# Kernel tuning notes

Hardware: AMD Instinct MI355X
Metric: run time of the kernel (lower is better)

Reference implementation:

```python
import jax, jax.numpy as jnp
import numpy as np

B, C, H, W = 16, 128, 128, 128
NUM_HEADS, HEAD_DIM = 4, 32
HIDDEN = NUM_HEADS * HEAD_DIM  # 128
GROUPS = 32
EPS = 1e-5


def setup_inputs() -> dict:
    key = jax.random.key(0)
    ks = jax.random.split(key, 6)
    # conv1x1 weights: torch Conv2d weight (out, in, 1, 1) -> stored as (out, in)
    fan_qkv = C
    fan_proj = HIDDEN
    return {
        "x": jax.random.normal(ks[0], (B, C, H, W), dtype=jnp.float32),
        "gn_w": jnp.ones((C,), dtype=jnp.float32),
        "gn_b": jnp.zeros((C,), dtype=jnp.float32),
        "qkv_w": jax.random.normal(ks[1], (3 * HIDDEN, C), dtype=jnp.float32) / np.sqrt(fan_qkv),
        "proj_w": jax.random.normal(ks[2], (C, HIDDEN), dtype=jnp.float32) / np.sqrt(fan_proj),
        "proj_b": jax.random.normal(ks[3], (C,), dtype=jnp.float32) * 0.01,
    }


def reference(x, gn_w, gn_b, qkv_w, proj_w, proj_b):
    b, c, h, w = x.shape
    n = h * w
    residual = x
    # GroupNorm(32 groups), biased variance, affine
    xg = x.reshape(b, GROUPS, c // GROUPS, h, w)
    mu = xg.mean(axis=(2, 3, 4), keepdims=True)
    var = xg.var(axis=(2, 3, 4), keepdims=True)
    xn = ((xg - mu) * jax.lax.rsqrt(var + EPS)).reshape(b, c, h, w)
    xn = xn * gn_w[None, :, None, None] + gn_b[None, :, None, None]
    # 1x1 conv QKV (no bias); channel layout -> (b, 3, heads, head_dim, n)
    qkv = jnp.einsum('oc,bchw->bohw', qkv_w, xn)
    qkv = qkv.reshape(b, 3, NUM_HEADS, HEAD_DIM, n)
    q, k, v = qkv[:, 0], qkv[:, 1], qkv[:, 2]
    q = jax.nn.softmax(q, axis=-1)   # over spatial positions
    k = jax.nn.softmax(k, axis=-2)   # over head_dim
    # context = k @ v^T : (b,h,D,D)
    ctx = jnp.einsum('bhdn,bhen->bhde', k, v)
    # out = context^T @ q : (b,h,D,n)
    out = jnp.einsum('bhde,bhdn->bhen', ctx, q)
    out = out.reshape(b, HIDDEN, h, w)
    # 1x1 conv projection (with bias)
    out = jnp.einsum('co,bohw->bchw', proj_w, out) + proj_b[None, :, None, None]
    return out + residual
```

## Files before the change

kernel.cpp:

```cpp
#include <hip/hip_runtime.h>


#define B_ 16
#define C_ 128
#define N_ 16384

typedef short bf16x8 __attribute__((ext_vector_type(8)));
typedef float f32x4 __attribute__((ext_vector_type(4)));
typedef unsigned u32x2 __attribute__((ext_vector_type(2)));

__device__ __forceinline__ ushort f2bf(float f) {
    union { float f; unsigned u; } v; v.f = f;
    unsigned r = (v.u + 0x7FFFu + ((v.u >> 16) & 1u)) >> 16;
    return (ushort)r;
}
__device__ __forceinline__ float bf2f(unsigned h) {
    union { unsigned u; float f; } v; v.u = h << 16;
    return v.f;
}

__global__ void k_pack(const float* __restrict__ w, ushort* __restrict__ wbf, int n) {
    int i = blockIdx.x * 256 + threadIdx.x;
    if (i < n) wbf[i] = f2bf(w[i]);
}

__global__ void k_stats(const float* __restrict__ x, const float* __restrict__ gnw,
                        const float* __restrict__ gnb, float* __restrict__ sc,
                        float* __restrict__ bi) {
    int bg = blockIdx.x;
    const float4* p = (const float4*)(x + (size_t)bg * (4 * N_));
    float s = 0.f, s2 = 0.f;
    for (int i = threadIdx.x; i < N_; i += 1024) {
        float4 v = p[i];
        s  += v.x + v.y + v.z + v.w;
        s2 += v.x * v.x + v.y * v.y + v.z * v.z + v.w * v.w;
    }
    #pragma unroll
    for (int d = 32; d > 0; d >>= 1) { s += __shfl_xor(s, d); s2 += __shfl_xor(s2, d); }
    __shared__ float ls[16], ls2[16];
    int wid = threadIdx.x >> 6, lane = threadIdx.x & 63;
    if (lane == 0) { ls[wid] = s; ls2[wid] = s2; }
    __syncthreads();
    if (threadIdx.x == 0) {
        float S = 0.f, S2 = 0.f;
        #pragma unroll
        for (int i = 0; i < 16; ++i) { S += ls[i]; S2 += ls2[i]; }
        float m = S / 65536.f;
        float var = S2 / 65536.f - m * m;
        float rs = rsqrtf(var + 1e-5f);
        int b = bg >> 5, g = bg & 31;
        #pragma unroll
        for (int i = 0; i < 4; ++i) {
            int c = g * 4 + i;
            float scv = rs * gnw[c];
            sc[b * 128 + c] = scv;
            bi[b * 128 + c] = gnb[c] - m * scv;
        }
    }
}


#define MFMA16(A, Bv, Cc) __builtin_amdgcn_mfma_f32_16x16x32_bf16(A, Bv, Cc, 0, 0, 0)

#define DO_Q(J, OT) do { \
    f32x4 acc = {0.f, 0.f, 0.f, 0.f}; \
    acc = MFMA16(wf[J][0], xb[0], acc); acc = MFMA16(wf[J][1], xb[1], acc); \
    acc = MFMA16(wf[J][2], xb[2], acc); acc = MFMA16(wf[J][3], xb[3], acc); \
    float e0 = __expf(acc[0]), e1 = __expf(acc[1]); \
    float e2 = __expf(acc[2]), e3 = __expf(acc[3]); \
    qacc[J][0] += e0; qacc[J][1] += e1; qacc[J][2] += e2; qacc[J][3] += e3; \
    u32x2 pkq; \
    pkq.x = (unsigned)f2bf(e0) | ((unsigned)f2bf(e1) << 16); \
    pkq.y = (unsigned)f2bf(e2) | ((unsigned)f2bf(e3) << 16); \
    *(u32x2*)(eqp + (OT) * 16) = pkq; \
} while (0)

#define DO_K(JLO, H) do { \
    f32x4 aL = {0.f, 0.f, 0.f, 0.f}, aH = {0.f, 0.f, 0.f, 0.f}; \
    aL = MFMA16(wf[JLO][0], xb[0], aL);     aH = MFMA16(wf[(JLO)+1][0], xb[0], aH); \
    aL = MFMA16(wf[JLO][1], xb[1], aL);     aH = MFMA16(wf[(JLO)+1][1], xb[1], aH); \
    aL = MFMA16(wf[JLO][2], xb[2], aL);     aH = MFMA16(wf[(JLO)+1][2], xb[2], aH); \
    aL = MFMA16(wf[JLO][3], xb[3], aL);     aH = MFMA16(wf[(JLO)+1][3], xb[3], aH); \
    float eL0 = __expf(aL[0]), eL1 = __expf(aL[1]), eL2 = __expf(aL[2]), eL3 = __expf(aL[3]); \
    float eH0 = __expf(aH[0]), eH1 = __expf(aH[1]), eH2 = __expf(aH[2]), eH3 = __expf(aH[3]); \
    float s = eL0 + eL1 + eL2 + eL3 + eH0 + eH1 + eH2 + eH3; \
    s += __shfl_xor(s, 16); s += __shfl_xor(s, 32); \
    float rinv = 1.f / s; \
    ksm[H][lg * 4 + 0][nloc] = f2bf(eL0 * rinv); \
    ksm[H][lg * 4 + 1][nloc] = f2bf(eL1 * rinv); \
    ksm[H][lg * 4 + 2][nloc] = f2bf(eL2 * rinv); \
    ksm[H][lg * 4 + 3][nloc] = f2bf(eL3 * rinv); \
    ksm[H][16 + lg * 4 + 0][nloc] = f2bf(eH0 * rinv); \
    ksm[H][16 + lg * 4 + 1][nloc] = f2bf(eH1 * rinv); \
    ksm[H][16 + lg * 4 + 2][nloc] = f2bf(eH2 * rinv); \
    ksm[H][16 + lg * 4 + 3][nloc] = f2bf(eH3 * rinv); \
} while (0)

#define DO_V(J, HV, EB) do { \
    f32x4 acc = {0.f, 0.f, 0.f, 0.f}; \
    acc = MFMA16(wf[J][0], xb[0], acc); acc = MFMA16(wf[J][1], xb[1], acc); \
    acc = MFMA16(wf[J][2], xb[2], acc); acc = MFMA16(wf[J][3], xb[3], acc); \
    vls[HV][(EB) + lg * 4 + 0][nloc] = f2bf(acc[0]); \
    vls[HV][(EB) + lg * 4 + 1][nloc] = f2bf(acc[1]); \
    vls[HV][(EB) + lg * 4 + 2][nloc] = f2bf(acc[2]); \
    vls[HV][(EB) + lg * 4 + 3][nloc] = f2bf(acc[3]); \
} while (0)

__global__ __launch_bounds__(256, 2) void k_main(
    const float* __restrict__ x, const ushort* __restrict__ wbf,
    const float* __restrict__ scA, const float* __restrict__ biA,
    ushort* __restrict__ eqT, float* __restrict__ qsumP, float* __restrict__ ctxP) {
    int blk = blockIdx.x;
    int b = blk >> 6, nb = blk & 63;
    int tid = threadIdx.x, wid = tid >> 6, lane = tid & 63;
    int l15 = lane & 15, lg = lane >> 4;

    __shared__ __align__(16) ushort xs[8192];
    __shared__ __align__(16) ushort ksm[4][32][72];
    __shared__ __align__(16) ushort vls[4][32][72];

    bf16x8 wf[6][4];
    {
        const ushort* wr = wbf + (size_t)(wid * 96 + l15) * 128 + lg * 8;
        #pragma unroll
        for (int j = 0; j < 6; ++j)
            #pragma unroll
            for (int kc = 0; kc < 4; ++kc)
                wf[j][kc] = *(const bf16x8*)(wr + j * 2048 + kc * 32);
    }

    float qacc[6][4];
    #pragma unroll
    for (int j = 0; j < 6; ++j)
        #pragma unroll
        for (int r = 0; r < 4; ++r) qacc[j][r] = 0.f;
    f32x4 cacc[2][2];
    #pragma unroll
    for (int di = 0; di < 2; ++di)
        #pragma unroll
        for (int ei = 0; ei < 2; ++ei) cacc[di][ei] = (f32x4){0.f, 0.f, 0.f, 0.f};

    const int pk_ = tid & 15, pcb = tid >> 4;
    const float* xrow = x + (size_t)b * (C_ * N_) + nb * 256 + pk_ * 4;
    float scv[8], biv[8];
    #pragma unroll
    for (int i = 0; i < 8; ++i) {
        scv[i] = scA[b * 128 + pcb * 8 + i];
        biv[i] = biA[b * 128 + pcb * 8 + i];
    }
    unsigned boffj[4];
    #pragma unroll
    for (int j = 0; j < 4; ++j) {
        int n = pk_ * 4 + j;
        boffj[j] = (unsigned)(n * 256 + ((pcb * 16) ^ ((n & 7) << 4)));
    }

    for (int ch = 0; ch < 4; ++ch) {
        union { uint4 v; unsigned w[4]; } wj0, wj1, wj2, wj3;
        #pragma unroll
        for (int i = 0; i < 8; ++i) {
            float4 v = *(const float4*)(xrow + (size_t)(pcb * 8 + i) * N_ + ch * 64);
            float s = scv[i], t = biv[i];
            unsigned e0 = f2bf(v.x * s + t), e1 = f2bf(v.y * s + t);
            unsigned e2 = f2bf(v.z * s + t), e3 = f2bf(v.w * s + t);
            int wI = i >> 1;
            if (i & 1) {
                wj0.w[wI] |= e0 << 16; wj1.w[wI] |= e1 << 16;
                wj2.w[wI] |= e2 << 16; wj3.w[wI] |= e3 << 16;
            } else {
                wj0.w[wI] = e0; wj1.w[wI] = e1; wj2.w[wI] = e2; wj3.w[wI] = e3;
            }
        }
        *(uint4*)((char*)xs + boffj[0]) = wj0.v;
        *(uint4*)((char*)xs + boffj[1]) = wj1.v;
        *(uint4*)((char*)xs + boffj[2]) = wj2.v;
        *(uint4*)((char*)xs + boffj[3]) = wj3.v;
        __syncthreads();

        for (int nt = 0; nt < 4; ++nt) {
            int row = nt * 16 + l15;
            bf16x8 xb[4];
            #pragma unroll
            for (int kc = 0; kc < 4; ++kc) {
                unsigned off = (unsigned)(row * 256 +
                    (((kc * 4 + lg) * 16) ^ ((row & 7) << 4)));
                xb[kc] = *(const bf16x8*)((const char*)xs + off);
            }
            int nloc = nt * 16 + l15;
            int ng = nb * 256 + ch * 64 + nloc;
            ushort* eqp = eqT + ((size_t)b * N_ + ng) * 128 + lg * 4;

            if (wid == 0) {
                DO_Q(0, 0); DO_Q(1, 1); DO_Q(2, 2); DO_Q(3, 3); DO_Q(4, 4); DO_Q(5, 5);
            } else if (wid == 1) {
                DO_Q(0, 6); DO_Q(1, 7); DO_K(2, 0); DO_K(4, 1);
            } else if (wid == 2) {
                DO_K(0, 2); DO_K(2, 3); DO_V(4, 0, 0); DO_V(5, 0, 16);
            } else {
                DO_V(0, 1, 0); DO_V(1, 1, 16); DO_V(2, 2, 0);
                DO_V(3, 2, 16); DO_V(4, 3, 0); DO_V(5, 3, 16);
            }
        }
        __syncthreads();

        #pragma unroll
        for (int ks = 0; ks < 2; ++ks) {
            bf16x8 A0 = *(const bf16x8*)&ksm[wid][l15][ks * 32 + lg * 8];
            bf16x8 A1 = *(const bf16x8*)&ksm[wid][16 + l15][ks * 32 + lg * 8];
            bf16x8 B0 = *(const bf16x8*)&vls[wid][l15][ks * 32 + lg * 8];
            bf16x8 B1 = *(const bf16x8*)&vls[wid][16 + l15][ks * 32 + lg * 8];
            cacc[0][0] = MFMA16(A0, B0, cacc[0][0]);
            cacc[0][1] = MFMA16(A0, B1, cacc[0][1]);
            cacc[1][0] = MFMA16(A1, B0, cacc[1][0]);
            cacc[1][1] = MFMA16(A1, B1, cacc[1][1]);
        }
        __syncthreads();
    }

    int nq = (wid == 0) ? 6 : (wid == 1 ? 2 : 0);
    #pragma unroll
    for (int j = 0; j < 6; ++j) {
        if (j < nq) {
            #pragma unroll
            for (int r = 0; r < 4; ++r) {
                float s = qacc[j][r];
                s += __shfl_xor(s, 1); s += __shfl_xor(s, 2);
                s += __shfl_xor(s, 4); s += __shfl_xor(s, 8);
                if (l15 == 0)
                    qsumP[(size_t)blk * 128 + (wid * 6 + j) * 16 + lg * 4 + r] = s;
            }
        }
    }
    float* cp = ctxP + (size_t)blk * 4096 + wid * 1024;
    #pragma unroll
    for (int di = 0; di < 2; ++di)
        #pragma unroll
        for (int ei = 0; ei < 2; ++ei)
            #pragma unroll
            for (int r = 0; r < 4; ++r)
                cp[(di * 16 + lg * 4 + r) * 32 + ei * 16 + l15] = cacc[di][ei][r];
}

__global__ void k_red(float* __restrict__ ctxP) {
    int blk = blockIdx.x;
    int b = blk >> 3, sl = blk & 7;
    float* base = ctxP + (size_t)b * 64 * 4096;
    #pragma unroll
    for (int r = 0; r < 2; ++r) {
        int i = sl * 512 + r * 256 + threadIdx.x;
        float s = 0.f;
        for (int q = 0; q < 64; ++q) s += base[(size_t)q * 4096 + i];
        base[i] = s;
    }
}

__global__ void k_comb(const float* __restrict__ ctxP, const float* __restrict__ qsumP,
                       const float* __restrict__ projw, ushort* __restrict__ mpp) {
    int b = blockIdx.x, tid = threadIdx.x;
    __shared__ float ctx[4096];
    __shared__ float qinv[128];
    for (int i = tid; i < 4096; i += 256)
        ctx[i] = ctxP[(size_t)b * 64 * 4096 + i];
    if (tid < 128) {
        float s = 0.f;
        const float* p = qsumP + (size_t)b * 64 * 128 + tid;
        for (int q = 0; q < 64; ++q) s += p[q * 128];
        qinv[tid] = 1.f / s;
    }
    __syncthreads();
    int c = tid >> 1, hd0 = (tid & 1) * 64;
    unsigned ow[32];
    for (int k = 0; k < 64; ++k) {
        int hd = hd0 + k, h = hd >> 5, d = hd & 31;
        const float* pw = projw + c * 128 + h * 32;
        const float* cx = ctx + h * 1024 + d * 32;
        float s = 0.f;
        #pragma unroll 8
        for (int e = 0; e < 32; ++e) s += pw[e] * cx[e];
        s *= qinv[hd];
        ushort bv = f2bf(s);
        if (k & 1) ow[k >> 1] |= ((unsigned)bv) << 16; else ow[k >> 1] = bv;
    }
    ushort* dst = mpp + ((size_t)(b * 128 + c)) * 128 + hd0;
    #pragma unroll
    for (int q = 0; q < 8; ++q) {
        uint4 t; t.x = ow[q * 4]; t.y = ow[q * 4 + 1]; t.z = ow[q * 4 + 2]; t.w = ow[q * 4 + 3];
        ((uint4*)dst)[q] = t;
    }
}

__global__ __launch_bounds__(256) void k_final(
    const ushort* __restrict__ eqT, const ushort* __restrict__ mpp,
    const float* __restrict__ projb, const float* __restrict__ x,
    float* __restrict__ out) {
    int blk = blockIdx.x;
    int b = blk >> 7, nb = blk & 127;
    int tid = threadIdx.x, wid = tid >> 6, lane = tid & 63;
    int l15 = lane & 15, lg = lane >> 4;

    __shared__ __align__(16) ushort att[16384];

    bf16x8 bm[2][4];
    #pragma unroll
    for (int ctk = 0; ctk < 2; ++ctk) {
        const ushort* br = mpp + ((size_t)(b * 128 + (wid * 2 + ctk) * 16 + l15)) * 128 + lg * 8;
        #pragma unroll
        for (int kc = 0; kc < 4; ++kc) bm[ctk][kc] = *(const bf16x8*)(br + kc * 32);
    }

    int n0 = nb * 128;
    #pragma unroll
    for (int nt = 0; nt < 8; ++nt) {
        const ushort* ar = eqT + ((size_t)b * N_ + n0 + nt * 16 + l15) * 128 + lg * 8;
        bf16x8 af[4];
        #pragma unroll
        for (int kc = 0; kc < 4; ++kc) af[kc] = *(const bf16x8*)(ar + kc * 32);
        #pragma unroll
        for (int ctk = 0; ctk < 2; ++ctk) {
            f32x4 a = {0.f, 0.f, 0.f, 0.f};
            #pragma unroll
            for (int kc = 0; kc < 4; ++kc) a = MFMA16(af[kc], bm[ctk][kc], a);
            int c = (wid * 2 + ctk) * 16 + l15;
            int nloc = nt * 16 + lg * 4;
            unsigned byte = (unsigned)(c * 256 + ((nloc * 2) ^ ((c & 15) << 4)));
            u32x2 pk;
            pk.x = (unsigned)f2bf(a[0]) | ((unsigned)f2bf(a[1]) << 16);
            pk.y = (unsigned)f2bf(a[2]) | ((unsigned)f2bf(a[3]) << 16);
            *(u32x2*)((char*)att + byte) = pk;
        }
    }
    __syncthreads();

    int crow = lane >> 5;
    int n4 = (lane & 31) * 4;
    #pragma unroll
    for (int it = 0; it < 16; ++it) {
        int c = wid * 32 + it * 2 + crow;
        unsigned byte = (unsigned)(c * 256 + ((n4 * 2) ^ ((c & 15) << 4)));
        u32x2 pk = *(const u32x2*)((const char*)att + byte);
        size_t off = (size_t)(b * C_ + c) * N_ + n0 + n4;
        f32x4 xv = __builtin_nontemporal_load((const f32x4*)(x + off));
        float pbv = projb[c];
        f32x4 o4;
        o4[0] = bf2f(pk.x & 0xffffu) + pbv + xv[0];
        o4[1] = bf2f(pk.x >> 16)     + pbv + xv[1];
        o4[2] = bf2f(pk.y & 0xffffu) + pbv + xv[2];
        o4[3] = bf2f(pk.y >> 16)     + pbv + xv[3];
        *(f32x4*)(out + off) = o4;
    }
}

extern "C" void kernel_launch(void* const* d_in, const int* in_sizes, int n_in,
                              void* d_out, int out_size, void* d_ws, size_t ws_size,
                              hipStream_t stream) {
    const float* x     = (const float*)d_in[0];
    const float* gnw   = (const float*)d_in[1];
    const float* gnb   = (const float*)d_in[2];
    const float* qkvw  = (const float*)d_in[3];
    const float* projw = (const float*)d_in[4];
    const float* projb = (const float*)d_in[5];
    float* out = (float*)d_out;

    char* ws = (char*)d_ws;
    ushort* wbf   = (ushort*)(ws);
    float*  qsumP = (float*)(ws + 102400);
    ushort* mpp   = (ushort*)(ws + 626688);
    float*  sc    = (float*)(ws + 626688);
    float*  bi    = (float*)(ws + 634880);
    float*  ctxP  = (float*)(ws + 1150976);
    ushort* eqT   = (ushort*)(ws + 17928192);

    k_pack <<<192,  256,  0, stream>>>(qkvw, wbf, 384 * 128);
    k_stats<<<512,  1024, 0, stream>>>(x, gnw, gnb, sc, bi);
    k_main <<<1024, 256,  0, stream>>>(x, wbf, sc, bi, eqT, qsumP, ctxP);
    k_red  <<<128,  256,  0, stream>>>(ctxP);
    k_comb <<<16,   256,  0, stream>>>(ctxP, qsumP, projw, mpp);
    k_final<<<2048, 256,  0, stream>>>(eqT, mpp, projb, x, out);
}
```

Baseline: 241.3 us.

## Fold weight packing into stats kernel and halve main-kernel LDS chunk size

The bf16 weight-packing kernel is merged into the GroupNorm stats kernel as extra blocks, removing one launch. The main kernel now processes 8 chunks of 32 positions instead of 4 chunks of 64, which roughly halves its LDS footprint (xs, ksm, vls) so more blocks can be resident per CU. The trailing barrier in each chunk is replaced by a barrier at the start of the next chunk. The cost is twice as many chunk iterations and barriers, with smaller global load batches per thread.

```diff
diff --git a/kernel.cpp b/kernel.cpp
--- a/kernel.cpp
+++ b/kernel.cpp
@@ -19,15 +19,16 @@
     return v.f;
 }
 
-__global__ void k_pack(const float* __restrict__ w, ushort* __restrict__ wbf, int n) {
-    int i = blockIdx.x * 256 + threadIdx.x;
-    if (i < n) wbf[i] = f2bf(w[i]);
-}
-
 __global__ void k_stats(const float* __restrict__ x, const float* __restrict__ gnw,
                         const float* __restrict__ gnb, float* __restrict__ sc,
-                        float* __restrict__ bi) {
+                        float* __restrict__ bi,
+                        const float* __restrict__ qkvw, ushort* __restrict__ wbf) {
     int bg = blockIdx.x;
+    if (bg >= 512) {
+        int i = (bg - 512) * 1024 + threadIdx.x;
+        if (i < 384 * 128) wbf[i] = f2bf(qkvw[i]);
+        return;
+    }
     const float4* p = (const float4*)(x + (size_t)bg * (4 * N_));
     float s = 0.f, s2 = 0.f;
     for (int i = threadIdx.x; i < N_; i += 1024) {
@@ -115,9 +116,9 @@
     int tid = threadIdx.x, wid = tid >> 6, lane = tid & 63;
     int l15 = lane & 15, lg = lane >> 4;
 
-    __shared__ __align__(16) ushort xs[8192];
-    __shared__ __align__(16) ushort ksm[4][32][72];
-    __shared__ __align__(16) ushort vls[4][32][72];
+    __shared__ __align__(16) ushort xs[4096];
+    __shared__ __align__(16) ushort ksm[4][32][40];
+    __shared__ __align__(16) ushort vls[4][32][40];
 
     bf16x8 wf[6][4];
     {
@@ -140,44 +141,44 @@
         #pragma unroll
         for (int ei = 0; ei < 2; ++ei) cacc[di][ei] = (f32x4){0.f, 0.f, 0.f, 0.f};
 
-    const int pk_ = tid & 15, pcb = tid >> 4;
+    const int pk_ = tid & 7, pcb = tid >> 3;
     const float* xrow = x + (size_t)b * (C_ * N_) + nb * 256 + pk_ * 4;
-    float scv[8], biv[8];
-    #pragma unroll
-    for (int i = 0; i < 8; ++i) {
-        scv[i] = scA[b * 128 + pcb * 8 + i];
-        biv[i] = biA[b * 128 + pcb * 8 + i];
+    float scv[4], biv[4];
+    #pragma unroll
+    for (int i = 0; i < 4; ++i) {
+        scv[i] = scA[b * 128 + pcb * 4 + i];
+        biv[i] = biA[b * 128 + pcb * 4 + i];
     }
     unsigned boffj[4];
     #pragma unroll
     for (int j = 0; j < 4; ++j) {
         int n = pk_ * 4 + j;
-        boffj[j] = (unsigned)(n * 256 + ((pcb * 16) ^ ((n & 7) << 4)));
-    }
-
-    for (int ch = 0; ch < 4; ++ch) {
-        union { uint4 v; unsigned w[4]; } wj0, wj1, wj2, wj3;
-        #pragma unroll
-        for (int i = 0; i < 8; ++i) {
-            float4 v = *(const float4*)(xrow + (size_t)(pcb * 8 + i) * N_ + ch * 64);
+        boffj[j] = (unsigned)(n * 256 + (((pcb >> 1) * 16) ^ ((n & 7) << 4)) + (pcb & 1) * 8);
+    }
+
+    for (int ch = 0; ch < 8; ++ch) {
+        __syncthreads();
+        unsigned e[4][4];
+        #pragma unroll
+        for (int i = 0; i < 4; ++i) {
+            float4 v = *(const float4*)(xrow + (size_t)(pcb * 4 + i) * N_ + ch * 32);
             float s = scv[i], t = biv[i];
-            unsigned e0 = f2bf(v.x * s + t), e1 = f2bf(v.y * s + t);
-            unsigned e2 = f2bf(v.z * s + t), e3 = f2bf(v.w * s + t);
-            int wI = i >> 1;
-            if (i & 1) {
-                wj0.w[wI] |= e0 << 16; wj1.w[wI] |= e1 << 16;
-                wj2.w[wI] |= e2 << 16; wj3.w[wI] |= e3 << 16;
-            } else {
-                wj0.w[wI] = e0; wj1.w[wI] = e1; wj2.w[wI] = e2; wj3.w[wI] = e3;
-            }
-        }
-        *(uint4*)((char*)xs + boffj[0]) = wj0.v;
-        *(uint4*)((char*)xs + boffj[1]) = wj1.v;
-        *(uint4*)((char*)xs + boffj[2]) = wj2.v;
-        *(uint4*)((char*)xs + boffj[3]) = wj3.v;
+            e[i][0] = f2bf(v.x * s + t);
+            e[i][1] = f2bf(v.y * s + t);
+            e[i][2] = f2bf(v.z * s + t);
+            e[i][3] = f2bf(v.w * s + t);
+        }
+        #pragma unroll
+        for (int j = 0; j < 4; ++j) {
+            u32x2 wj;
+            wj.x = e[0][j] | (e[1][j] << 16);
+            wj.y = e[2][j] | (e[3][j] << 16);
+            *(u32x2*)((char*)xs + boffj[j]) = wj;
+        }
         __syncthreads();
 
-        for (int nt = 0; nt < 4; ++nt) {
+        #pragma unroll
+        for (int nt = 0; nt < 2; ++nt) {
             int row = nt * 16 + l15;
             bf16x8 xb[4];
             #pragma unroll
@@ -187,7 +188,7 @@
                 xb[kc] = *(const bf16x8*)((const char*)xs + off);
             }
             int nloc = nt * 16 + l15;
-            int ng = nb * 256 + ch * 64 + nloc;
+            int ng = nb * 256 + ch * 32 + nloc;
             ushort* eqp = eqT + ((size_t)b * N_ + ng) * 128 + lg * 4;
 
             if (wid == 0) {
@@ -203,18 +204,16 @@
         }
         __syncthreads();
 
-        #pragma unroll
-        for (int ks = 0; ks < 2; ++ks) {
-            bf16x8 A0 = *(const bf16x8*)&ksm[wid][l15][ks * 32 + lg * 8];
-            bf16x8 A1 = *(const bf16x8*)&ksm[wid][16 + l15][ks * 32 + lg * 8];
-            bf16x8 B0 = *(const bf16x8*)&vls[wid][l15][ks * 32 + lg * 8];
-            bf16x8 B1 = *(const bf16x8*)&vls[wid][16 + l15][ks * 32 + lg * 8];
+        {
+            bf16x8 A0 = *(const bf16x8*)&ksm[wid][l15][lg * 8];
+            bf16x8 A1 = *(const bf16x8*)&ksm[wid][16 + l15][lg * 8];
+            bf16x8 B0 = *(const bf16x8*)&vls[wid][l15][lg * 8];
+            bf16x8 B1 = *(const bf16x8*)&vls[wid][16 + l15][lg * 8];
             cacc[0][0] = MFMA16(A0, B0, cacc[0][0]);
             cacc[0][1] = MFMA16(A0, B1, cacc[0][1]);
             cacc[1][0] = MFMA16(A1, B0, cacc[1][0]);
             cacc[1][1] = MFMA16(A1, B1, cacc[1][1]);
         }
-        __syncthreads();
     }
 
     int nq = (wid == 0) ? 6 : (wid == 1 ? 2 : 0);
@@ -370,8 +369,7 @@
     float*  ctxP  = (float*)(ws + 1150976);
     ushort* eqT   = (ushort*)(ws + 17928192);
 
-    k_pack <<<192,  256,  0, stream>>>(qkvw, wbf, 384 * 128);
-    k_stats<<<512,  1024, 0, stream>>>(x, gnw, gnb, sc, bi);
+    k_stats<<<560,  1024, 0, stream>>>(x, gnw, gnb, sc, bi, qkvw, wbf);
     k_main <<<1024, 256,  0, stream>>>(x, wbf, sc, bi, eqT, qsumP, ctxP);
     k_red  <<<128,  256,  0, stream>>>(ctxP);
     k_comb <<<16,   256,  0, stream>>>(ctxP, qsumP, projw, mpp);
```

Result: faster. 234.8 us (-2.7%).
